# Kernel optimization log

Hardware: AMD Instinct MI355X
Metric: run time of the kernel (lower is better)

## Reference

```python
import jax, jax.numpy as jnp
import numpy as np

ALPHA = 0.5
BETA = 0.5
SMOOTH = 1e-08


def setup_inputs() -> dict:
    key = jax.random.key(0)
    k1, k2 = jax.random.split(key)
    B, C, H, W = 8, 19, 512, 512
    pred = jax.random.normal(k1, (B, C, H, W), dtype=jnp.float32)
    target = jax.random.randint(k2, (B, H, W), 0, C, dtype=jnp.int32)
    return {"pred": pred, "target": target}


def reference(pred, target):
    B, C, H, W = pred.shape
    p = jax.nn.softmax(pred, axis=1)                       # [B,C,H,W]
    # one-hot target along class axis: [B,C,H,W]
    t = (target[:, None, :, :] == jnp.arange(C, dtype=target.dtype)[None, :, None, None]).astype(p.dtype)
    tp = jnp.einsum('bchw,bchw->bc', p, t)                 # true positives
    sum_p = jnp.sum(p, axis=(2, 3))                        # [B,C]
    sum_t = jnp.sum(t, axis=(2, 3))                        # [B,C]
    fp = sum_p - tp
    fn = sum_t - tp
    tversky = (tp + SMOOTH) / (tp + ALPHA * fp + BETA * fn + SMOOTH)
    return jnp.mean(1.0 - tversky)
```

## Files before the change

kernel.cpp:

```cpp
#include <hip/hip_runtime.h>

#define NC 19
#define NB 8
#define HW (512 * 512)
#define SMOOTH 1e-8f
#define THREADS 256
#define GROUPS 2
#define NBC (NB * NC)


__global__ __launch_bounds__(THREADS) void tversky_pass1(
        const float* __restrict__ pred, const int* __restrict__ tgt,
        float* __restrict__ acc) {
    const int b   = blockIdx.y;
    const int tid = threadIdx.x;

    float a1[NC], a2[NC];
#pragma unroll
    for (int c = 0; c < NC; ++c) { a1[c] = 0.0f; a2[c] = 0.0f; }

    const float* pb = pred + (size_t)b * NC * HW;
    const int*   tb = tgt  + (size_t)b * HW;

    const int block_base = blockIdx.x * (THREADS * 4 * GROUPS);

#pragma unroll
    for (int g = 0; g < GROUPS; ++g) {
        const int px = block_base + (g * THREADS + tid) * 4;
        const float* pp = pb + px;

        float sx = 0.0f, sy = 0.0f, sz = 0.0f, sw = 0.0f;
#pragma unroll
        for (int c = 0; c < NC; ++c) {
            const float4 v = *(const float4*)(pp + (size_t)c * HW);
            sx += __expf(v.x); sy += __expf(v.y);
            sz += __expf(v.z); sw += __expf(v.w);
        }
        const float ivx = 1.0f / sx, ivy = 1.0f / sy;
        const float ivz = 1.0f / sz, ivw = 1.0f / sw;

        asm volatile("" ::: "memory");

        const int4 t = *(const int4*)(tb + px);

#pragma unroll
        for (int c = 0; c < NC; ++c) {
            const float4 v = *(const float4*)(pp + (size_t)c * HW);
            const float ex = __expf(v.x) * ivx;
            const float ey = __expf(v.y) * ivy;
            const float ez = __expf(v.z) * ivz;
            const float ew = __expf(v.w) * ivw;
            const bool mx = (t.x == c), my = (t.y == c);
            const bool mz = (t.z == c), mw = (t.w == c);
            a2[c] += (mx ? ex : 0.0f) + (my ? ey : 0.0f)
                   + (mz ? ez : 0.0f) + (mw ? ew : 0.0f);
            a1[c] += ((ex + ey) + (ez + ew))
                   + ((mx ? 1.0f : 0.0f) + (my ? 1.0f : 0.0f)
                    + (mz ? 1.0f : 0.0f) + (mw ? 1.0f : 0.0f));
        }
    }

#pragma unroll
    for (int c = 0; c < NC; ++c) {
#pragma unroll
        for (int off = 1; off < 64; off <<= 1) {
            a1[c] += __shfl_xor(a1[c], off, 64);
            a2[c] += __shfl_xor(a2[c], off, 64);
        }
    }

    __shared__ float lds[4][2 * NC];
    const int wave = tid >> 6;
    if ((tid & 63) == 0) {
#pragma unroll
        for (int c = 0; c < NC; ++c) {
            lds[wave][c]      = a2[c];
            lds[wave][NC + c] = a1[c];
        }
    }
    __syncthreads();
    if (tid < 2 * NC) {
        const float s = lds[0][tid] + lds[1][tid] + lds[2][tid] + lds[3][tid];
        const int c = (tid < NC) ? tid : (tid - NC);
        float* dst = (tid < NC) ? acc : (acc + NBC);
        atomicAdd(&dst[b * NC + c], s);
    }
}

__global__ __launch_bounds__(256) void tversky_pass2(const float* __restrict__ acc,
                                                     float* __restrict__ out) {
    __shared__ float red[256];
    const int i = threadIdx.x;
    float v = 0.0f;
    if (i < NBC) {
        const float tp  = acc[i];
        const float spc = acc[NBC + i];
        const float tv = (tp + SMOOTH) / (0.5f * spc + SMOOTH);
        v = 1.0f - tv;
    }
    red[i] = v;
    __syncthreads();
    for (int s = 128; s > 0; s >>= 1) {
        if (i < s) red[i] += red[i + s];
        __syncthreads();
    }
    if (i == 0) out[0] = red[0] / (float)NBC;
}

extern "C" void kernel_launch(void* const* d_in, const int* in_sizes, int n_in,
                              void* d_out, int out_size, void* d_ws, size_t ws_size,
                              hipStream_t stream) {
    const float* pred = (const float*)d_in[0];
    const int*   tgt  = (const int*)d_in[1];
    float* acc = (float*)d_ws;
    float* out = (float*)d_out;

    hipMemsetAsync(acc, 0, 2 * NBC * sizeof(float), stream);

    dim3 grid(HW / (THREADS * 4 * GROUPS), NB);
    tversky_pass1<<<grid, THREADS, 0, stream>>>(pred, tgt, acc);

    tversky_pass2<<<1, 256, 0, stream>>>(acc, out);
}
```

Before: 235.0 us.

## Shrink per-thread work and accumulate true positives via LDS atomics

Each thread now handles 2 pixels instead of 8, with float2 loads and a grid four times larger, and launch_bounds asks for 8 blocks per CU. The true positive and target count are no longer kept as per-class select accumulators. Each thread captures the exp of its target class during the first pass and adds it to shared-memory bins with LDS atomics. This cuts the register and ALU cost of the second pass and halves the shuffle reductions, in exchange for LDS atomic contention, more blocks and more global atomics.

```diff
diff --git a/kernel.cpp b/kernel.cpp
--- a/kernel.cpp
+++ b/kernel.cpp
@@ -5,85 +5,75 @@
 #define HW (512 * 512)
 #define SMOOTH 1e-8f
 #define THREADS 256
-#define GROUPS 2
+#define PXT 2
 #define NBC (NB * NC)
 
 
-__global__ __launch_bounds__(THREADS) void tversky_pass1(
+__global__ __launch_bounds__(THREADS, 8) void tversky_pass1(
         const float* __restrict__ pred, const int* __restrict__ tgt,
         float* __restrict__ acc) {
     const int b   = blockIdx.y;
     const int tid = threadIdx.x;
 
-    float a1[NC], a2[NC];
-#pragma unroll
-    for (int c = 0; c < NC; ++c) { a1[c] = 0.0f; a2[c] = 0.0f; }
+    __shared__ float lds_tp[NC];
+    __shared__ float lds_ct[NC];
+    __shared__ float lds_red[THREADS / 64][NC];
+
+    if (tid < NC) { lds_tp[tid] = 0.0f; lds_ct[tid] = 0.0f; }
+    __syncthreads();
 
     const float* pb = pred + (size_t)b * NC * HW;
     const int*   tb = tgt  + (size_t)b * HW;
 
-    const int block_base = blockIdx.x * (THREADS * 4 * GROUPS);
+    const int px = blockIdx.x * (THREADS * PXT) + tid * PXT;
+    const float* pp = pb + px;
+    const int2 t = *(const int2*)(tb + px);
 
+    float sx = 0.0f, sy = 0.0f, etx = 0.0f, ety = 0.0f;
 #pragma unroll
-    for (int g = 0; g < GROUPS; ++g) {
-        const int px = block_base + (g * THREADS + tid) * 4;
-        const float* pp = pb + px;
+    for (int c = 0; c < NC; ++c) {
+        const float2 v = *(const float2*)(pp + (size_t)c * HW);
+        const float ex = __expf(v.x), ey = __expf(v.y);
+        sx += ex; sy += ey;
+        etx = (t.x == c) ? ex : etx;
+        ety = (t.y == c) ? ey : ety;
+    }
+    const float ivx = 1.0f / sx, ivy = 1.0f / sy;
 
-        float sx = 0.0f, sy = 0.0f, sz = 0.0f, sw = 0.0f;
+    atomicAdd(&lds_tp[t.x], etx * ivx);
+    atomicAdd(&lds_tp[t.y], ety * ivy);
+    atomicAdd(&lds_ct[t.x], 1.0f);
+    atomicAdd(&lds_ct[t.y], 1.0f);
+
+    asm volatile("" ::: "memory");
+
+    float a1[NC];
 #pragma unroll
-        for (int c = 0; c < NC; ++c) {
-            const float4 v = *(const float4*)(pp + (size_t)c * HW);
-            sx += __expf(v.x); sy += __expf(v.y);
-            sz += __expf(v.z); sw += __expf(v.w);
-        }
-        const float ivx = 1.0f / sx, ivy = 1.0f / sy;
-        const float ivz = 1.0f / sz, ivw = 1.0f / sw;
-
-        asm volatile("" ::: "memory");
-
-        const int4 t = *(const int4*)(tb + px);
-
-#pragma unroll
-        for (int c = 0; c < NC; ++c) {
-            const float4 v = *(const float4*)(pp + (size_t)c * HW);
-            const float ex = __expf(v.x) * ivx;
-            const float ey = __expf(v.y) * ivy;
-            const float ez = __expf(v.z) * ivz;
-            const float ew = __expf(v.w) * ivw;
-            const bool mx = (t.x == c), my = (t.y == c);
-            const bool mz = (t.z == c), mw = (t.w == c);
-            a2[c] += (mx ? ex : 0.0f) + (my ? ey : 0.0f)
-                   + (mz ? ez : 0.0f) + (mw ? ew : 0.0f);
-            a1[c] += ((ex + ey) + (ez + ew))
-                   + ((mx ? 1.0f : 0.0f) + (my ? 1.0f : 0.0f)
-                    + (mz ? 1.0f : 0.0f) + (mw ? 1.0f : 0.0f));
-        }
+    for (int c = 0; c < NC; ++c) {
+        const float2 v = *(const float2*)(pp + (size_t)c * HW);
+        a1[c] = __expf(v.x) * ivx + __expf(v.y) * ivy;
     }
 
 #pragma unroll
     for (int c = 0; c < NC; ++c) {
 #pragma unroll
-        for (int off = 1; off < 64; off <<= 1) {
+        for (int off = 1; off < 64; off <<= 1)
             a1[c] += __shfl_xor(a1[c], off, 64);
-            a2[c] += __shfl_xor(a2[c], off, 64);
-        }
     }
 
-    __shared__ float lds[4][2 * NC];
     const int wave = tid >> 6;
     if ((tid & 63) == 0) {
 #pragma unroll
-        for (int c = 0; c < NC; ++c) {
-            lds[wave][c]      = a2[c];
-            lds[wave][NC + c] = a1[c];
-        }
+        for (int c = 0; c < NC; ++c) lds_red[wave][c] = a1[c];
     }
     __syncthreads();
-    if (tid < 2 * NC) {
-        const float s = lds[0][tid] + lds[1][tid] + lds[2][tid] + lds[3][tid];
-        const int c = (tid < NC) ? tid : (tid - NC);
-        float* dst = (tid < NC) ? acc : (acc + NBC);
-        atomicAdd(&dst[b * NC + c], s);
+
+    if (tid < NC) {
+        float sum_p = 0.0f;
+#pragma unroll
+        for (int w = 0; w < THREADS / 64; ++w) sum_p += lds_red[w][tid];
+        atomicAdd(&acc[b * NC + tid], lds_tp[tid]);
+        atomicAdd(&acc[NBC + b * NC + tid], sum_p + lds_ct[tid]);
     }
 }
 
@@ -117,7 +107,7 @@
 
     hipMemsetAsync(acc, 0, 2 * NBC * sizeof(float), stream);
 
-    dim3 grid(HW / (THREADS * 4 * GROUPS), NB);
+    dim3 grid(HW / (THREADS * PXT), NB);
     tversky_pass1<<<grid, THREADS, 0, stream>>>(pred, tgt, acc);
 
     tversky_pass2<<<1, 256, 0, stream>>>(acc, out);
```

After: 242.8 us. 1.03x slower.
